# Kernel tuning notes

Hardware: AMD Instinct MI355X
Metric: run time of the kernel (lower is better)

The kernel has to match this reference:

```python
import jax, jax.numpy as jnp
import numpy as np

B, T, D, G, E, V = 32, 1024, 512, 256, 8, 8192


def setup_inputs() -> dict:
    key = jax.random.key(0)
    k1, k2, k3, k4, k5 = jax.random.split(key, 5)
    return {
        "gate_features": jax.random.normal(k1, (B, G), dtype=jnp.float32),
        "input_features": jax.random.normal(k2, (B, T, D), dtype=jnp.float32),
        "Wg": jax.random.normal(k3, (G, E), dtype=jnp.float32) * 0.02,
        "bg": jnp.zeros((E,), dtype=jnp.float32),
        "We": jax.random.normal(k4, (E, D, V), dtype=jnp.float32) * 0.02,
        "be": jnp.zeros((E, V), dtype=jnp.float32),
        "target_ids": jax.random.randint(k5, (B, T), 0, V, dtype=jnp.int64),
    }


def reference(gate_features, input_features, Wg, bg, We, be, target_ids):
    # ---- Router: linear gate -> softmax probs -> top-1 assignment ----
    router_logits = gate_features @ Wg + bg            # [B, E]
    probs = jax.nn.softmax(router_logits, axis=-1)     # [B, E]
    assignments = jnp.argmax(router_logits, axis=-1)   # [B]

    # ---- Dispatch: gather each sample's expert parameters ----
    W_sel = We[assignments]                            # [B, D, V]
    b_sel = be[assignments]                            # [B, V]

    # ---- Expert compute: linear LM head + cross-entropy loss ----
    logits = jnp.einsum("btd,bdv->btv", input_features, W_sel) + b_sel[:, None, :]
    logp = jax.nn.log_softmax(logits, axis=-1)         # [B, T, V]
    nll = -jnp.take_along_axis(logp, target_ids[..., None], axis=-1)[..., 0]  # [B, T]
    ce_per_sample = nll.mean(axis=-1)                  # [B]

    # ---- Combine: total_loss = sum over experts of per-expert mean loss ----
    sums = jax.ops.segment_sum(ce_per_sample, assignments, num_segments=E)   # [E]
    counts = jax.ops.segment_sum(jnp.ones_like(ce_per_sample), assignments, num_segments=E)
    loss_per_expert = jnp.where(counts > 0, sums / jnp.maximum(counts, 1.0), 0.0)
    total_loss = loss_per_expert.sum()

    return total_loss, assignments, probs
```

## Files before the change

### kernel.cpp

```cpp
#include <hip/hip_runtime.h>

#define NB 32
#define NT 1024
#define ND 512
#define NG 256
#define NE 8
#define NV 8192
#define NROW (NB * NT)

#define XBF_BYTES   (33554432)
#define WT_BYTES    (67108864)
#define PSUM_BYTES  (8388608)
#define TL_BYTES    (131072)

#define BM2 256
#define BN2 256
#define NCT (NV / BN2)

typedef float f32x4 __attribute__((ext_vector_type(4)));
typedef __bf16 bf16x8 __attribute__((ext_vector_type(8)));
typedef unsigned int u32_g __attribute__((address_space(1)));
typedef unsigned int u32_l __attribute__((address_space(3)));
typedef unsigned short ushort_t;

__device__ __forceinline__ void g2l16(void* lds, const void* g) {
    __builtin_amdgcn_global_load_lds((const u32_g*)g, (u32_l*)lds, 16, 0, 0);
}

__device__ __forceinline__ unsigned short f2bf(float f) {
    unsigned int u = __float_as_uint(f);
    unsigned int r = (u + 0x7fffu + ((u >> 16) & 1u)) >> 16;
    return (unsigned short)r;
}

__global__ void k_router(const float* __restrict__ gate, const float* __restrict__ Wg,
                         const float* __restrict__ bg, float* __restrict__ out,
                         int* __restrict__ assign, int* __restrict__ counts) {
    __shared__ float lg[NB][NE];
    __shared__ int lam[NB];
    int tid = threadIdx.x;
    int b = tid >> 3, e = tid & 7;
    float acc = bg[e];
    const float* gr = gate + b * NG;
    for (int g = 0; g < NG; ++g) acc = fmaf(gr[g], Wg[g * NE + e], acc);
    lg[b][e] = acc;
    __syncthreads();
    if (tid < NB) {
        float mx = lg[tid][0]; int am = 0;
        for (int j = 1; j < NE; ++j) { float v = lg[tid][j]; if (v > mx) { mx = v; am = j; } }
        float den = 0.f, ex[NE];
        for (int j = 0; j < NE; ++j) { ex[j] = __expf(lg[tid][j] - mx); den += ex[j]; }
        float inv = 1.f / den;
        for (int j = 0; j < NE; ++j) out[1 + NB + tid * NE + j] = ex[j] * inv;
        out[1 + tid] = (float)am;
        assign[tid] = am;
        lam[tid] = am;
    }
    __syncthreads();
    if (tid == 0) {
        int c[NE] = {0,0,0,0,0,0,0,0};
        for (int i = 0; i < NB; ++i) c[lam[i]]++;
        for (int j = 0; j < NE; ++j) counts[j] = c[j];
        out[0] = 0.f;
    }
}

__global__ void k_convx(const float4* __restrict__ in, ushort_t* __restrict__ out, int n4) {
    int i = blockIdx.x * blockDim.x + threadIdx.x;
    int stride = gridDim.x * blockDim.x;
    for (; i < n4; i += stride) {
        float4 v = in[i];
        ushort4 o;
        o.x = f2bf(v.x); o.y = f2bf(v.y); o.z = f2bf(v.z); o.w = f2bf(v.w);
        ((ushort4*)out)[i] = o;
    }
}

__global__ void k_transw(const float* __restrict__ We, ushort_t* __restrict__ Wt) {
    __shared__ float tile[32][33];
    int e = blockIdx.z, d0 = blockIdx.y * 32, v0 = blockIdx.x * 32;
    int tx = threadIdx.x & 31, ty = threadIdx.x >> 5;
    const float* src = We + (size_t)e * ND * NV;
    for (int j = 0; j < 4; ++j)
        tile[ty + j * 8][tx] = src[(size_t)(d0 + ty + j * 8) * NV + v0 + tx];
    __syncthreads();
    ushort_t* dst = Wt + (size_t)e * NV * ND;
    for (int j = 0; j < 4; ++j)
        dst[(size_t)(v0 + ty + j * 8) * ND + d0 + tx] = f2bf(tile[tx][ty + j * 8]);
}


#define BAR_MID() do { \
    asm volatile("" ::: "memory"); \
    __builtin_amdgcn_s_barrier(); \
    asm volatile("s_waitcnt lgkmcnt(0)" ::: "memory"); \
    __builtin_amdgcn_sched_barrier(0); } while (0)

#define BAR_END() do { \
    asm volatile("" ::: "memory"); \
    __builtin_amdgcn_s_barrier(); \
    asm volatile("" ::: "memory"); } while (0)

#define MFMA_QUAD(MH, NH) do { \
    __builtin_amdgcn_s_setprio(1); \
    _Pragma("unroll") \
    for (int m_ = 0; m_ < 4; ++m_) \
      _Pragma("unroll") \
      for (int n_ = 0; n_ < 2; ++n_) \
        _Pragma("unroll") \
        for (int ks_ = 0; ks_ < 2; ++ks_) \
          acc[(MH) * 4 + m_][(NH) * 2 + n_] = __builtin_amdgcn_mfma_f32_16x16x32_bf16( \
              af[m_][ks_], bfr[(NH) * 2 + n_][ks_], acc[(MH) * 4 + m_][(NH) * 2 + n_], 0, 0, 0); \
    __builtin_amdgcn_s_setprio(0); } while (0)

__global__ __launch_bounds__(512, 2)
void k_gemm(const ushort_t* __restrict__ Xbf, const ushort_t* __restrict__ Wtbf,
            const float* __restrict__ be, const int* __restrict__ assign,
            float* __restrict__ psum) {
    __shared__ alignas(16) char smem[135168];
    float* lws = (float*)(smem + 131072);

    const int tid  = threadIdx.x;
    const int wid  = tid >> 6, lane = tid & 63;
    const int q = lane >> 4, ln = lane & 15;
    const int wr = wid >> 2, wc = wid & 3;

    const int bid = blockIdx.x;
    const int wg  = ((bid & 7) << 9) | (bid >> 3);
    const int ct  = wg >> 7;
    const int rt  = wg & 127;
    const int e   = assign[rt >> 2];
    const size_t eV = (size_t)e * NV;

    const int rquo = tid >> 3;
    const int scol = ((tid & 7) ^ (rquo & 7)) << 3;
    const ushort_t* gA = Xbf + (size_t)(rt * BM2 + rquo) * ND + scol;
    const ushort_t* gB = Wtbf + (eV + ct * BN2 + rquo) * ND + scol;
    char* ldsW = smem + wid * 1024;
    const int axor = ln & 7;

    f32x4 acc[8][4];
#pragma unroll
    for (int i = 0; i < 8; ++i)
#pragma unroll
        for (int j = 0; j < 4; ++j) acc[i][j] = (f32x4){0.f, 0.f, 0.f, 0.f};

#define STA(KT, BP, H) do { \
    char* d_ = ldsW + (BP) * 65536 + (H) * 16384; \
    const ushort_t* g_ = gA + (size_t)(H) * 128 * ND + (KT) * 64; \
    g2l16(d_, g_); g2l16(d_ + 8192, g_ + (size_t)64 * ND); } while (0)

#define STB(KT, BP, H) do { \
    char* d_ = ldsW + (BP) * 65536 + 32768 + (H) * 16384; \
    const ushort_t* g_ = gB + (size_t)(H) * 128 * ND + (KT) * 64; \
    g2l16(d_, g_); g2l16(d_ + 8192, g_ + (size_t)64 * ND); } while (0)

#define RDA(BP, MF, KS) \
    (*(const bf16x8*)(smem + (BP) * 65536 + wr * 16384 + \
                      ((MF) * 16 + ln) * 128 + ((((KS) * 4 + q) ^ axor) << 4)))

#define RDB(BP, NF, KS) \
    (*(const bf16x8*)(smem + (BP) * 65536 + 32768 + (wc >> 1) * 16384 + \
                      (((wc & 1) * 64 + (NF) * 16 + ln) * 128) + ((((KS) * 4 + q) ^ axor) << 4)))

    STB(0, 0, 0); STB(0, 0, 1); STA(0, 0, 0); STA(0, 0, 1);
    STB(1, 1, 0); STB(1, 1, 1);
    asm volatile("s_waitcnt vmcnt(4)" ::: "memory");
    __builtin_amdgcn_s_barrier();
    asm volatile("" ::: "memory");

    bf16x8 af[4][2];
    bf16x8 bfr[4][2];

#pragma unroll
    for (int kt = 0; kt < 8; ++kt) {
        const int p = kt & 1, np = p ^ 1;

#pragma unroll
        for (int m = 0; m < 4; ++m) { af[m][0] = RDA(p, m, 0); af[m][1] = RDA(p, m, 1); }
#pragma unroll
        for (int n = 0; n < 2; ++n) { bfr[n][0] = RDB(p, n, 0); bfr[n][1] = RDB(p, n, 1); }
        if (kt < 7) STA(kt + 1, np, 0);
        BAR_MID();
        MFMA_QUAD(0, 0);
        BAR_END();

#pragma unroll
        for (int n = 0; n < 2; ++n) { bfr[2 + n][0] = RDB(p, 2 + n, 0); bfr[2 + n][1] = RDB(p, 2 + n, 1); }
        if (kt < 7) STA(kt + 1, np, 1);
        BAR_MID();
        MFMA_QUAD(0, 1);
        BAR_END();

#pragma unroll
        for (int m = 0; m < 4; ++m) { af[m][0] = RDA(p, 4 + m, 0); af[m][1] = RDA(p, 4 + m, 1); }
        if (kt < 6) STB(kt + 2, p, 0);
        BAR_MID();
        MFMA_QUAD(1, 1);
        BAR_END();

        if (kt < 6) STB(kt + 2, p, 1);
        BAR_MID();
        MFMA_QUAD(1, 0);
        if (kt < 6)       { asm volatile("s_waitcnt vmcnt(4)" ::: "memory"); }
        else if (kt == 6) { asm volatile("s_waitcnt vmcnt(0)" ::: "memory"); }
        BAR_END();
    }

    const float LOG2E = 1.44269504088896f;
    float partial[32];
#pragma unroll
    for (int i = 0; i < 32; ++i) partial[i] = 0.f;
#pragma unroll
    for (int nf = 0; nf < 4; ++nf) {
        int col = (ct << 8) + (wc << 6) + nf * 16 + ln;
        float eb = be[eV + col] * LOG2E;
#pragma unroll
        for (int mf = 0; mf < 8; ++mf)
#pragma unroll
            for (int r = 0; r < 4; ++r)
                partial[mf * 4 + r] += exp2f(fmaf(acc[mf][nf][r], LOG2E, eb));
    }
#pragma unroll
    for (int i = 0; i < 32; ++i) {
        float pv = partial[i];
        pv += __shfl_xor(pv, 1); pv += __shfl_xor(pv, 2);
        pv += __shfl_xor(pv, 4); pv += __shfl_xor(pv, 8);
        partial[i] = pv;
    }
    if (ln == 0) {
#pragma unroll
        for (int mf = 0; mf < 8; ++mf)
#pragma unroll
            for (int r = 0; r < 4; ++r)
                lws[wid * 128 + mf * 16 + q * 4 + r] = partial[mf * 4 + r];
    }
    __syncthreads();
    if (tid < 256) {
        int wrh = tid >> 7, idx = tid & 127;
        float s = lws[(wrh * 4 + 0) * 128 + idx] + lws[(wrh * 4 + 1) * 128 + idx]
                + lws[(wrh * 4 + 2) * 128 + idx] + lws[(wrh * 4 + 3) * 128 + idx];
        psum[(size_t)ct * NROW + rt * 256 + tid] = s;
    }
#undef STA
#undef STB
#undef RDA
#undef RDB
}

__global__ void k_target(const ushort_t* __restrict__ Xbf, const ushort_t* __restrict__ Wtbf,
                         const float* __restrict__ be, const int* __restrict__ assign,
                         const int* __restrict__ tgt, float* __restrict__ tl) {
    int wave = threadIdx.x >> 6, lane = threadIdx.x & 63;
    int wg = blockIdx.x * 4 + wave;
    int b = wg >> 10, t = wg & 1023;
    int e = assign[b];
    int id = tgt[b * NT + t];
    const bf16x8 xv = *(const bf16x8*)(Xbf + (size_t)(b * NT + t) * ND + lane * 8);
    const bf16x8 wv = *(const bf16x8*)(Wtbf + ((size_t)e * NV + id) * ND + lane * 8);
    float s = 0.f;
#pragma unroll
    for (int i = 0; i < 8; ++i) s = fmaf((float)xv[i], (float)wv[i], s);
    for (int off = 32; off; off >>= 1) s += __shfl_down(s, off);
    if (lane == 0) tl[b * NT + t] = s + be[(size_t)e * NV + id];
}

__global__ void k_loss(const float* __restrict__ psum, const float* __restrict__ tl,
                       float* __restrict__ nll) {
    int b = blockIdx.x, tid = threadIdx.x;
    float acc = 0.f;
#pragma unroll
    for (int j = 0; j < 4; ++j) {
        int t = j * 256 + tid;
        float s = 0.f;
        for (int ct = 0; ct < NCT; ++ct) s += psum[(size_t)ct * NROW + b * NT + t];
        acc += __logf(s) - tl[b * NT + t];
    }
    __shared__ float red[4];
    for (int off = 32; off; off >>= 1) acc += __shfl_down(acc, off);
    if ((tid & 63) == 0) red[tid >> 6] = acc;
    __syncthreads();
    if (tid == 0) nll[b] = red[0] + red[1] + red[2] + red[3];
}

__global__ void k_final(const float* __restrict__ nll_sum, const int* __restrict__ assign,
                        const int* __restrict__ counts, float* __restrict__ out) {
    int tid = threadIdx.x;
    float contrib = 0.f;
    if (tid < NB) {
        float ce = nll_sum[tid] * (1.0f / (float)NT);
        contrib = ce / (float)counts[assign[tid]];
    }
    for (int off = 32; off; off >>= 1) contrib += __shfl_down(contrib, off);
    if (tid == 0) out[0] = contrib;
}

extern "C" void kernel_launch(void* const* d_in, const int* in_sizes, int n_in,
                              void* d_out, int out_size, void* d_ws, size_t ws_size,
                              hipStream_t stream) {
    const float* gate = (const float*)d_in[0];
    const float* X    = (const float*)d_in[1];
    const float* Wg   = (const float*)d_in[2];
    const float* bg   = (const float*)d_in[3];
    const float* We   = (const float*)d_in[4];
    const float* be   = (const float*)d_in[5];
    const int*   tgt  = (const int*)d_in[6];
    float* out = (float*)d_out;

    char* ws = (char*)d_ws;
    ushort_t* Xbf  = (ushort_t*)ws;
    ushort_t* Wtbf = (ushort_t*)(ws + XBF_BYTES);
    float*    psum = (float*)(ws + XBF_BYTES + WT_BYTES);
    float*    tl   = (float*)(ws + XBF_BYTES + WT_BYTES + PSUM_BYTES);
    int*      assign = (int*)(ws + XBF_BYTES + WT_BYTES + PSUM_BYTES + TL_BYTES);
    int*      counts = assign + 32;
    float*    nll    = (float*)(assign + 64);

    k_router<<<1, 256, 0, stream>>>(gate, Wg, bg, out, assign, counts);
    k_convx<<<4096, 256, 0, stream>>>((const float4*)X, Xbf, NB * NT * ND / 4);
    k_transw<<<dim3(NV / 32, ND / 32, NE), 256, 0, stream>>>(We, Wtbf);
    k_gemm<<<(NROW / BM2) * (NV / BN2), 512, 0, stream>>>(Xbf, Wtbf, be, assign, psum);
    k_target<<<NB * NT / 4, 256, 0, stream>>>(Xbf, Wtbf, be, assign, tgt, tl);
    k_loss<<<NB, 256, 0, stream>>>(psum, tl, nll);
    k_final<<<1, 64, 0, stream>>>(nll, assign, counts, out);
}
```

Baseline: 599.4 us.

## Make GEMM persistent with cross-tile prefetch and vectorize weight transpose

```diff
diff --git a/kernel.cpp b/kernel.cpp
--- a/kernel.cpp
+++ b/kernel.cpp
@@ -19,6 +19,7 @@
 
 typedef float f32x4 __attribute__((ext_vector_type(4)));
 typedef __bf16 bf16x8 __attribute__((ext_vector_type(8)));
+typedef unsigned short ushort8_v __attribute__((ext_vector_type(8)));
 typedef unsigned int u32_g __attribute__((address_space(1)));
 typedef unsigned int u32_l __attribute__((address_space(3)));
 typedef unsigned short ushort_t;
@@ -77,16 +78,31 @@
 }
 
 __global__ void k_transw(const float* __restrict__ We, ushort_t* __restrict__ Wt) {
-    __shared__ float tile[32][33];
-    int e = blockIdx.z, d0 = blockIdx.y * 32, v0 = blockIdx.x * 32;
-    int tx = threadIdx.x & 31, ty = threadIdx.x >> 5;
-    const float* src = We + (size_t)e * ND * NV;
-    for (int j = 0; j < 4; ++j)
-        tile[ty + j * 8][tx] = src[(size_t)(d0 + ty + j * 8) * NV + v0 + tx];
+    __shared__ float tile[64][68];
+    int e = blockIdx.z, d0 = blockIdx.y * 64, v0 = blockIdx.x * 64;
+    int tid = threadIdx.x;
+    const float* src = We + (size_t)e * ND * NV + (size_t)d0 * NV + v0;
+    int dr = tid >> 4;
+    int c4 = tid & 15;
+#pragma unroll
+    for (int j = 0; j < 4; ++j) {
+        int d = dr + 16 * j;
+        float4 v = *(const float4*)(src + (size_t)d * NV + c4 * 4);
+        *(float4*)&tile[d][((c4 ^ (d >> 3)) & 15) * 4] = v;
+    }
     __syncthreads();
-    ushort_t* dst = Wt + (size_t)e * NV * ND;
-    for (int j = 0; j < 4; ++j)
-        dst[(size_t)(v0 + ty + j * 8) * ND + d0 + tx] = f2bf(tile[tx][ty + j * 8]);
+    ushort_t* dst = Wt + (size_t)e * NV * ND + (size_t)v0 * ND + d0;
+    int vr = tid >> 3;
+    int t8 = tid & 7;
+#pragma unroll
+    for (int j = 0; j < 2; ++j) {
+        int v = vr + 32 * j;
+        ushort8_v o;
+#pragma unroll
+        for (int i = 0; i < 8; ++i)
+            o[i] = f2bf(tile[t8 * 8 + i][(((v >> 2) ^ t8) & 15) * 4 + (v & 3)]);
+        *(ushort8_v*)(dst + (size_t)v * ND + t8 * 8) = o;
+    }
 }
 
 
@@ -125,34 +141,27 @@
     const int q = lane >> 4, ln = lane & 15;
     const int wr = wid >> 2, wc = wid & 3;
 
-    const int bid = blockIdx.x;
-    const int wg  = ((bid & 7) << 9) | (bid >> 3);
-    const int ct  = wg >> 7;
-    const int rt  = wg & 127;
-    const int e   = assign[rt >> 2];
-    const size_t eV = (size_t)e * NV;
+    const int pid  = blockIdx.x;
+    const int xcd  = pid & 7;
+    const int base = pid >> 3;
 
     const int rquo = tid >> 3;
     const int scol = ((tid & 7) ^ (rquo & 7)) << 3;
-    const ushort_t* gA = Xbf + (size_t)(rt * BM2 + rquo) * ND + scol;
-    const ushort_t* gB = Wtbf + (eV + ct * BN2 + rquo) * ND + scol;
+    const ushort_t* gAl = Xbf  + (size_t)rquo * ND + scol;
+    const ushort_t* gBl = Wtbf + (size_t)rquo * ND + scol;
     char* ldsW = smem + wid * 1024;
     const int axor = ln & 7;
 
     f32x4 acc[8][4];
-#pragma unroll
-    for (int i = 0; i < 8; ++i)
-#pragma unroll
-        for (int j = 0; j < 4; ++j) acc[i][j] = (f32x4){0.f, 0.f, 0.f, 0.f};
-
-#define STA(KT, BP, H) do { \
+
+#define STA(OFF, KT, BP, H) do { \
     char* d_ = ldsW + (BP) * 65536 + (H) * 16384; \
-    const ushort_t* g_ = gA + (size_t)(H) * 128 * ND + (KT) * 64; \
+    const ushort_t* g_ = gAl + (OFF) + (H) * 128 * ND + (KT) * 64; \
     g2l16(d_, g_); g2l16(d_ + 8192, g_ + (size_t)64 * ND); } while (0)
 
-#define STB(KT, BP, H) do { \
+#define STB(OFF, KT, BP, H) do { \
     char* d_ = ldsW + (BP) * 65536 + 32768 + (H) * 16384; \
-    const ushort_t* g_ = gB + (size_t)(H) * 128 * ND + (KT) * 64; \
+    const ushort_t* g_ = gBl + (OFF) + (H) * 128 * ND + (KT) * 64; \
     g2l16(d_, g_); g2l16(d_ + 8192, g_ + (size_t)64 * ND); } while (0)
 
 #define RDA(BP, MF, KS) \
@@ -163,84 +172,119 @@
     (*(const bf16x8*)(smem + (BP) * 65536 + 32768 + (wc >> 1) * 16384 + \
                       (((wc & 1) * 64 + (NF) * 16 + ln) * 128) + ((((KS) * 4 + q) ^ axor) << 4)))
 
-    STB(0, 0, 0); STB(0, 0, 1); STA(0, 0, 0); STA(0, 0, 1);
-    STB(1, 1, 0); STB(1, 1, 1);
-    asm volatile("s_waitcnt vmcnt(4)" ::: "memory");
-    __builtin_amdgcn_s_barrier();
-    asm volatile("" ::: "memory");
+    {
+        int wg0 = (xcd << 9) | base;
+        int rt0 = wg0 & 127, ct0 = wg0 >> 7;
+        int e0  = assign[rt0 >> 2];
+        int oA  = rt0 * (BM2 * ND);
+        int oB  = (e0 * NV + ct0 * BN2) * ND;
+        STB(oB, 0, 0, 0); STB(oB, 0, 0, 1); STA(oA, 0, 0, 0); STA(oA, 0, 0, 1);
+        STB(oB, 1, 1, 0); STB(oB, 1, 1, 1);
+        asm volatile("s_waitcnt vmcnt(4)" ::: "memory");
+        __builtin_amdgcn_s_barrier();
+        asm volatile("" ::: "memory");
+    }
 
     bf16x8 af[4][2];
     bf16x8 bfr[4][2];
 
-#pragma unroll
-    for (int kt = 0; kt < 8; ++kt) {
-        const int p = kt & 1, np = p ^ 1;
-
-#pragma unroll
-        for (int m = 0; m < 4; ++m) { af[m][0] = RDA(p, m, 0); af[m][1] = RDA(p, m, 1); }
-#pragma unroll
-        for (int n = 0; n < 2; ++n) { bfr[n][0] = RDB(p, n, 0); bfr[n][1] = RDB(p, n, 1); }
-        if (kt < 7) STA(kt + 1, np, 0);
-        BAR_MID();
-        MFMA_QUAD(0, 0);
+#pragma unroll 1
+    for (int tt = 0; tt < 16; ++tt) {
+        const int wg  = (xcd << 9) | (base + 32 * tt);
+        const int ct  = wg >> 7, rt = wg & 127;
+        const int e   = assign[rt >> 2];
+        const int oAc = rt * (BM2 * ND);
+        const int oBc = (e * NV + ct * BN2) * ND;
+        const size_t eV = (size_t)e * NV;
+        const int wgn = (xcd << 9) | ((base + 32 * (tt + 1)) & 511);
+        const int ctn = wgn >> 7, rtn = wgn & 127;
+        const int en  = assign[rtn >> 2];
+        const int oAn = rtn * (BM2 * ND);
+        const int oBn = (en * NV + ctn * BN2) * ND;
+        const bool more = (tt < 15);
+
+#pragma unroll
+        for (int i = 0; i < 8; ++i)
+#pragma unroll
+            for (int j = 0; j < 4; ++j) acc[i][j] = (f32x4){0.f, 0.f, 0.f, 0.f};
+
+#pragma unroll
+        for (int kt = 0; kt < 8; ++kt) {
+            const int p = kt & 1, np = p ^ 1;
+
+#pragma unroll
+            for (int m = 0; m < 4; ++m) { af[m][0] = RDA(p, m, 0); af[m][1] = RDA(p, m, 1); }
+#pragma unroll
+            for (int n = 0; n < 2; ++n) { bfr[n][0] = RDB(p, n, 0); bfr[n][1] = RDB(p, n, 1); }
+            if (kt < 7)      STA(oAc, kt + 1, np, 0);
+            else if (more)   STA(oAn, 0, np, 0);
+            BAR_MID();
+            MFMA_QUAD(0, 0);
+            BAR_END();
+
+#pragma unroll
+            for (int n = 0; n < 2; ++n) { bfr[2 + n][0] = RDB(p, 2 + n, 0); bfr[2 + n][1] = RDB(p, 2 + n, 1); }
+            if (kt < 7)      STA(oAc, kt + 1, np, 1);
+            else if (more)   STA(oAn, 0, np, 1);
+            BAR_MID();
+            MFMA_QUAD(0, 1);
+            BAR_END();
+
+#pragma unroll
+            for (int m = 0; m < 4; ++m) { af[m][0] = RDA(p, 4 + m, 0); af[m][1] = RDA(p, 4 + m, 1); }
+            if (kt < 6)      STB(oBc, kt + 2, p, 0);
+            else if (more)   STB(oBn, kt - 6, p, 0);
+            BAR_MID();
+            MFMA_QUAD(1, 1);
+            BAR_END();
+
+            if (kt < 6)      STB(oBc, kt + 2, p, 1);
+            else if (more)   STB(oBn, kt - 6, p, 1);
+            BAR_MID();
+            MFMA_QUAD(1, 0);
+            if (kt < 6 || more) { asm volatile("s_waitcnt vmcnt(4)" ::: "memory"); }
+            else if (kt == 6)   { asm volatile("s_waitcnt vmcnt(0)" ::: "memory"); }
+            BAR_END();
+        }
+
+        const float LOG2E = 1.44269504088896f;
+        float partial[32];
+#pragma unroll
+        for (int i = 0; i < 32; ++i) partial[i] = 0.f;
+#pragma unroll
+        for (int nf = 0; nf < 4; ++nf) {
+            int col = (ct << 8) + (wc << 6) + nf * 16 + ln;
+            float eb = be[eV + col] * LOG2E;
+#pragma unroll
+            for (int mf = 0; mf < 8; ++mf)
+#pragma unroll
+                for (int r = 0; r < 4; ++r)
+                    partial[mf * 4 + r] += exp2f(fmaf(acc[mf][nf][r], LOG2E, eb));
+        }
+#pragma unroll
+        for (int i = 0; i < 32; ++i) {
+            float pv = partial[i];
+            pv += __shfl_xor(pv, 1); pv += __shfl_xor(pv, 2);
+            pv += __shfl_xor(pv, 4); pv += __shfl_xor(pv, 8);
+            partial[i] = pv;
+        }
+        if (ln == 0) {
+#pragma unroll
+            for (int mf = 0; mf < 8; ++mf)
+#pragma unroll
+                for (int r = 0; r < 4; ++r)
+                    lws[wid * 128 + mf * 16 + q * 4 + r] = partial[mf * 4 + r];
+        }
+        asm volatile("s_waitcnt lgkmcnt(0)" ::: "memory");
+        __builtin_amdgcn_s_barrier();
+        asm volatile("" ::: "memory");
+        if (tid < 256) {
+            int wrh = tid >> 7, idx = tid & 127;
+            float s = lws[(wrh * 4 + 0) * 128 + idx] + lws[(wrh * 4 + 1) * 128 + idx]
+                    + lws[(wrh * 4 + 2) * 128 + idx] + lws[(wrh * 4 + 3) * 128 + idx];
+            psum[(size_t)ct * NROW + rt * 256 + tid] = s;
+        }
         BAR_END();
-
-#pragma unroll
-        for (int n = 0; n < 2; ++n) { bfr[2 + n][0] = RDB(p, 2 + n, 0); bfr[2 + n][1] = RDB(p, 2 + n, 1); }
-        if (kt < 7) STA(kt + 1, np, 1);
-        BAR_MID();
-        MFMA_QUAD(0, 1);
-        BAR_END();
-
-#pragma unroll
-        for (int m = 0; m < 4; ++m) { af[m][0] = RDA(p, 4 + m, 0); af[m][1] = RDA(p, 4 + m, 1); }
-        if (kt < 6) STB(kt + 2, p, 0);
-        BAR_MID();
-        MFMA_QUAD(1, 1);
-        BAR_END();
-
-        if (kt < 6) STB(kt + 2, p, 1);
-        BAR_MID();
-        MFMA_QUAD(1, 0);
-        if (kt < 6)       { asm volatile("s_waitcnt vmcnt(4)" ::: "memory"); }
-        else if (kt == 6) { asm volatile("s_waitcnt vmcnt(0)" ::: "memory"); }
-        BAR_END();
-    }
-
-    const float LOG2E = 1.44269504088896f;
-    float partial[32];
-#pragma unroll
-    for (int i = 0; i < 32; ++i) partial[i] = 0.f;
-#pragma unroll
-    for (int nf = 0; nf < 4; ++nf) {
-        int col = (ct << 8) + (wc << 6) + nf * 16 + ln;
-        float eb = be[eV + col] * LOG2E;
-#pragma unroll
-        for (int mf = 0; mf < 8; ++mf)
-#pragma unroll
-            for (int r = 0; r < 4; ++r)
-                partial[mf * 4 + r] += exp2f(fmaf(acc[mf][nf][r], LOG2E, eb));
-    }
-#pragma unroll
-    for (int i = 0; i < 32; ++i) {
-        float pv = partial[i];
-        pv += __shfl_xor(pv, 1); pv += __shfl_xor(pv, 2);
-        pv += __shfl_xor(pv, 4); pv += __shfl_xor(pv, 8);
-        partial[i] = pv;
-    }
-    if (ln == 0) {
-#pragma unroll
-        for (int mf = 0; mf < 8; ++mf)
-#pragma unroll
-            for (int r = 0; r < 4; ++r)
-                lws[wid * 128 + mf * 16 + q * 4 + r] = partial[mf * 4 + r];
-    }
-    __syncthreads();
-    if (tid < 256) {
-        int wrh = tid >> 7, idx = tid & 127;
-        float s = lws[(wrh * 4 + 0) * 128 + idx] + lws[(wrh * 4 + 1) * 128 + idx]
-                + lws[(wrh * 4 + 2) * 128 + idx] + lws[(wrh * 4 + 3) * 128 + idx];
-        psum[(size_t)ct * NROW + rt * 256 + tid] = s;
     }
 #undef STA
 #undef STB
@@ -318,8 +362,8 @@
 
     k_router<<<1, 256, 0, stream>>>(gate, Wg, bg, out, assign, counts);
     k_convx<<<4096, 256, 0, stream>>>((const float4*)X, Xbf, NB * NT * ND / 4);
-    k_transw<<<dim3(NV / 32, ND / 32, NE), 256, 0, stream>>>(We, Wtbf);
-    k_gemm<<<(NROW / BM2) * (NV / BN2), 512, 0, stream>>>(Xbf, Wtbf, be, assign, psum);
+    k_transw<<<dim3(NV / 64, ND / 64, NE), 256, 0, stream>>>(We, Wtbf);
+    k_gemm<<<256, 512, 0, stream>>>(Xbf, Wtbf, be, assign, psum);
     k_target<<<NB * NT / 4, 256, 0, stream>>>(Xbf, Wtbf, be, assign, tgt, tl);
     k_loss<<<NB, 256, 0, stream>>>(psum, tl, nll);
     k_final<<<1, 64, 0, stream>>>(nll, assign, counts, out);
```

Result: slower. 719.9 us (+20.1%).
